# Performance work log

Hardware: AMD Instinct MI355X
Metric: run time of the kernel (lower is better)

Reference implementation:

```python
import jax, jax.numpy as jnp
import numpy as np

GROUP = 64      # quantization group size along the K (in_features) dim
QMAX = 7.0      # symmetric signed int4 range [-7, 7]


def fake_quant_w4a4(t):
    """Per-group symmetric int4 fake-quantization along last dim (STE-friendly).

    t: [..., K] with K % GROUP == 0. Emulates nunchaku's quantize_w4a4
    numerics: scale = max|group| / 7, q = clip(round(t/scale)) * scale.
    """
    shp = t.shape
    g = t.reshape(shp[:-1] + (shp[-1] // GROUP, GROUP))
    scale = jnp.maximum(jnp.max(jnp.abs(g), axis=-1, keepdims=True) / QMAX, 1e-8)
    q = jnp.clip(jnp.round(g / scale), -QMAX, QMAX) * scale
    # straight-through estimator so gradients flow through the quant branch
    q = g + jax.lax.stop_gradient(q - g)
    return q.reshape(shp)


def setup_inputs() -> dict:
    key = jax.random.key(0)
    k0, k1, k2, k3, k4, k5 = jax.random.split(key, 6)
    B, K, N, R = 8192, 2048, 2048, 32  # tokens, in_features, out_features, rank
    x = jax.random.normal(k0, (B, K), jnp.float32)
    residual_weight = jax.random.normal(k1, (N, K), jnp.float32) * 0.02
    lora_down = jax.random.normal(k2, (K, R), jnp.float32) * 0.02
    lora_up = jax.random.normal(k3, (N, R), jnp.float32) * 0.02
    smooth = jax.random.uniform(k4, (K,), jnp.float32, minval=0.5, maxval=2.0)
    bias = jax.random.normal(k5, (N,), jnp.float32) * 0.01
    return {"x": x, "residual_weight": residual_weight, "lora_down": lora_down,
            "lora_up": lora_up, "smooth": smooth, "bias": bias}


def reference(x, residual_weight, lora_down, lora_up, smooth, bias):
    """SVDQuant forward: W4A4 GEMM on the residual weight fused with an
    FP low-rank (SVD) correction and per-channel smoothing.

    y = Q4(x*smooth) @ Q4(W_res).T + (x*smooth) @ lora_down @ lora_up.T + bias
    """
    x_s = x * smooth                                   # [B, K] smoothed activations
    y_lr = (x_s @ lora_down) @ lora_up.T               # [B, R] -> [B, N] low-rank branch
    y_q = fake_quant_w4a4(x_s) @ fake_quant_w4a4(residual_weight).T  # int4xint4 branch
    return y_q + y_lr + bias
```

## Files before the change

kernel.cpp:

```cpp
#include <hip/hip_runtime.h>
#include <stdint.h>


typedef __attribute__((ext_vector_type(8))) short short8;
typedef __attribute__((ext_vector_type(8))) unsigned short ushort8;
typedef __attribute__((ext_vector_type(4))) unsigned short ushort4v;
typedef __attribute__((ext_vector_type(4))) float floatx4;

#define M_TOK 8192
#define K_IN  2048
#define N_OUT 2048
#define RANK  32
#define KC    2080
#define NKT   65
#define XS_STRIDE 2056

__device__ __forceinline__ unsigned short f2bf(float f) {
  unsigned int u = __float_as_uint(f);
  u += 0x7fff + ((u >> 16) & 1);
  return (unsigned short)(u >> 16);
}

__device__ __forceinline__ void quant8(const float* v, unsigned short* q) {
  float amax = 0.f;
#pragma unroll
  for (int i = 0; i < 8; ++i) amax = fmaxf(amax, fabsf(v[i]));
  amax = fmaxf(amax, __shfl_xor(amax, 1, 64));
  amax = fmaxf(amax, __shfl_xor(amax, 2, 64));
  amax = fmaxf(amax, __shfl_xor(amax, 4, 64));
  float scale = fmaxf(amax / 7.0f, 1e-8f);
#pragma unroll
  for (int i = 0; i < 8; ++i) {
    float qq = rintf(v[i] / scale);
    qq = fminf(fmaxf(qq, -7.f), 7.f);
    q[i] = f2bf(qq * scale);
  }
}

__global__ __launch_bounds__(256) void ldt_kernel(const float* __restrict__ ld,
                                                  unsigned short* __restrict__ ldT) {
  int t = threadIdx.x, b = blockIdx.x;
  int r = t & 31, kk = b * 64 + (t >> 5);
#pragma unroll
  for (int i = 0; i < 8; ++i)
    ldT[r * 2048 + kk + i * 8] = f2bf(ld[(size_t)(kk + i * 8) * RANK + r]);
}

__global__ __launch_bounds__(256) void prep_kernel(const float* __restrict__ x,
                                                   const float* __restrict__ smooth,
                                                   const float* __restrict__ wgt,
                                                   const unsigned short* __restrict__ ldT,
                                                   const float* __restrict__ lup,
                                                   unsigned short* __restrict__ Xcat,
                                                   unsigned short* __restrict__ Wcat) {
  __shared__ unsigned short xs[16 * XS_STRIDE];
  __shared__ float red[4][16][32];
  int tid = threadIdx.x;

  if (blockIdx.x >= 512) {
    int row = blockIdx.x - 512;
    const float4* wr = (const float4*)(wgt + (size_t)row * K_IN);
    float4 a0 = wr[tid * 2], a1 = wr[tid * 2 + 1];
    float v[8] = {a0.x, a0.y, a0.z, a0.w, a1.x, a1.y, a1.z, a1.w};
    ushort8 q;
    quant8(v, (unsigned short*)&q);
    *(ushort8*)(Wcat + (size_t)row * KC + tid * 8) = q;
    if (tid < 32) Wcat[(size_t)row * KC + 2048 + tid] = f2bf(lup[row * RANK + tid]);
    return;
  }

  int rowbase = blockIdx.x * 16;
  int w = tid >> 6, lane = tid & 63, quad = lane >> 4, l16 = lane & 15;

  const float4* sr = (const float4*)smooth;
  float4 s0 = sr[tid * 2], s1 = sr[tid * 2 + 1];
#pragma unroll 2
  for (int r = 0; r < 16; ++r) {
    const float4* xr = (const float4*)(x + (size_t)(rowbase + r) * K_IN);
    float4 a0 = xr[tid * 2], a1 = xr[tid * 2 + 1];
    float v[8] = {a0.x * s0.x, a0.y * s0.y, a0.z * s0.z, a0.w * s0.w,
                  a1.x * s1.x, a1.y * s1.y, a1.z * s1.z, a1.w * s1.w};
    ushort8 q;
    quant8(v, (unsigned short*)&q);
    *(ushort8*)(Xcat + (size_t)(rowbase + r) * KC + tid * 8) = q;
    ushort8 sb;
#pragma unroll
    for (int t = 0; t < 8; ++t) sb[t] = f2bf(v[t]);
    *(ushort8*)(xs + r * XS_STRIDE + tid * 8) = sb;
  }
  __syncthreads();

  floatx4 acc[2];
  acc[0] = (floatx4)0.f;
  acc[1] = (floatx4)0.f;
  int kbase = w * 512;
#pragma unroll 2
  for (int it = 0; it < 16; ++it) {
    int k = kbase + it * 32 + quad * 8;
    short8 af = *(const short8*)(xs + l16 * XS_STRIDE + k);
    short8 b0 = *(const short8*)(ldT + (size_t)l16 * 2048 + k);
    short8 b1 = *(const short8*)(ldT + (size_t)(16 + l16) * 2048 + k);
    acc[0] = __builtin_amdgcn_mfma_f32_16x16x32_bf16(af, b0, acc[0], 0, 0, 0);
    acc[1] = __builtin_amdgcn_mfma_f32_16x16x32_bf16(af, b1, acc[1], 0, 0, 0);
  }
#pragma unroll
  for (int nt = 0; nt < 2; ++nt)
#pragma unroll
    for (int r = 0; r < 4; ++r)
      red[w][quad * 4 + r][nt * 16 + l16] = acc[nt][r];
  __syncthreads();
  if (tid < 128) {
    int rl = tid >> 3, seg = tid & 7;
    ushort4v o;
#pragma unroll
    for (int j = 0; j < 4; ++j) {
      int c = seg * 4 + j;
      float s = red[0][rl][c] + red[1][rl][c] + red[2][rl][c] + red[3][rl][c];
      o[j] = f2bf(s);
    }
    *(ushort4v*)(Xcat + (size_t)(rowbase + rl) * KC + 2048 + seg * 4) = o;
  }
}

__device__ __forceinline__ void gld_lds16(const unsigned short* g, unsigned short* l) {
  __builtin_amdgcn_global_load_lds(
      (const __attribute__((address_space(1))) unsigned int*)g,
      (__attribute__((address_space(3))) unsigned int*)l, 16, 0, 0);
}

__global__ __launch_bounds__(512) void gemm_kernel(const unsigned short* __restrict__ Xcat,
                                                   const unsigned short* __restrict__ Wcat,
                                                   const float* __restrict__ bias,
                                                   float* __restrict__ out) {
  __shared__ unsigned short smem[49152];
  int tid = threadIdx.x;
  int w = tid >> 6, lane = tid & 63, quad = lane >> 4, l16 = lane & 15;
  int wm = w >> 2, wn = w & 3;

  int bid = blockIdx.x;
  int wg = (bid & 7) * 32 + (bid >> 3);
  int bM = (wg >> 3) * 256;
  int bN = (wg & 7) * 256;

  int rowA = tid >> 2;
  int csrc = (tid & 3) ^ ((tid >> 3) & 3);
  const unsigned short* Ag = Xcat + (size_t)(bM + rowA) * KC + csrc * 8;
  const unsigned short* Bg = Wcat + (size_t)(bN + rowA) * KC + csrc * 8;
  int ldsA = w * 512;
  int ldsB = 8192 + w * 512;

#define STAGE(k0, cbuf)                                                      \
  do {                                                                       \
    gld_lds16(Ag + (k0),            smem + (cbuf) + ldsA);                   \
    gld_lds16(Ag + 128 * KC + (k0), smem + (cbuf) + 4096 + ldsA);            \
    gld_lds16(Bg + (k0),            smem + (cbuf) + ldsB);                   \
    gld_lds16(Bg + 128 * KC + (k0), smem + (cbuf) + 4096 + ldsB);            \
  } while (0)

  int cx = (quad ^ ((l16 >> 1) & 3)) * 8;
  int aoff = (wm * 128 + l16) * 32 + cx;
  int boff = 8192 + (wn * 64 + l16) * 32 + cx;

  floatx4 acc[8][4];
#pragma unroll
  for (int mt = 0; mt < 8; ++mt)
#pragma unroll
    for (int nt = 0; nt < 4; ++nt) acc[mt][nt] = (floatx4)0.f;

  int c0 = 0, c1 = 16384, c2 = 32768;

  STAGE(0, c0);
  STAGE(32, c1);
  asm volatile("s_waitcnt vmcnt(4)" ::: "memory");
  __builtin_amdgcn_s_barrier();

  for (int t = 0; t < NKT; ++t) {
    if (t + 2 < NKT) STAGE((t + 2) * 32, c2);

    short8 a[8], b[4];
#pragma unroll
    for (int mt = 0; mt < 8; ++mt) a[mt] = *(const short8*)(smem + c0 + aoff + mt * 512);
#pragma unroll
    for (int nt = 0; nt < 4; ++nt) b[nt] = *(const short8*)(smem + c0 + boff + nt * 512);

    __builtin_amdgcn_s_setprio(1);
#pragma unroll
    for (int mt = 0; mt < 8; ++mt)
#pragma unroll
      for (int nt = 0; nt < 4; ++nt)
        acc[mt][nt] = __builtin_amdgcn_mfma_f32_16x16x32_bf16(a[mt], b[nt],
                                                              acc[mt][nt], 0, 0, 0);
    __builtin_amdgcn_s_setprio(0);

    if (t < NKT - 2)
      asm volatile("s_waitcnt vmcnt(4)" ::: "memory");
    else
      asm volatile("s_waitcnt vmcnt(0)" ::: "memory");
    __builtin_amdgcn_s_barrier();
    int tmp = c0; c0 = c1; c1 = c2; c2 = tmp;
  }
#undef STAGE

#pragma unroll
  for (int nt = 0; nt < 4; ++nt) {
    int col = bN + wn * 64 + nt * 16 + l16;
    float bv = bias[col];
#pragma unroll
    for (int mt = 0; mt < 8; ++mt) {
      int row = bM + wm * 128 + mt * 16 + quad * 4;
#pragma unroll
      for (int r2 = 0; r2 < 4; ++r2)
        out[(size_t)(row + r2) * N_OUT + col] = acc[mt][nt][r2] + bv;
    }
  }
}

extern "C" void kernel_launch(void* const* d_in, const int* in_sizes, int n_in,
                              void* d_out, int out_size, void* d_ws, size_t ws_size,
                              hipStream_t stream) {
  const float* x      = (const float*)d_in[0];
  const float* wgt    = (const float*)d_in[1];
  const float* ld     = (const float*)d_in[2];
  const float* lup    = (const float*)d_in[3];
  const float* smooth = (const float*)d_in[4];
  const float* bias   = (const float*)d_in[5];
  float* out = (float*)d_out;

  unsigned short* Xcat = (unsigned short*)d_ws;
  unsigned short* Wcat = Xcat + (size_t)M_TOK * KC;
  unsigned short* ldT  = Wcat + (size_t)N_OUT * KC;

  hipLaunchKernelGGL(ldt_kernel, dim3(K_IN / 64), dim3(256), 0, stream, ld, ldT);
  hipLaunchKernelGGL(prep_kernel, dim3(512 + N_OUT), dim3(256), 0, stream,
                     x, smooth, wgt, ldT, lup, Xcat, Wcat);
  hipLaunchKernelGGL(gemm_kernel, dim3((M_TOK / 256) * (N_OUT / 256)), dim3(512), 0, stream,
                     Xcat, Wcat, bias, out);
}
```

Before: 214.4 us.

## Use 64-wide K tiles with double buffering and ping-pong interleaved MFMA phases

The GEMM K tile grows from 32 to 64, so the concatenated K dimension is padded to 2112 with zeroed tail columns written by the prep kernel. Staging moves to two 64KB buffers with an 8-way XOR swizzle. The loop body is split into four barrier-separated phases that load fragments and then issue MFMAs under raised priority, in a ping-pong style meant to overlap LDS reads and compute across waves. The aim is fewer loop iterations and less barrier/wait overhead per FLOP. The cost is more LDS use, which limits occupancy, many extra barriers, and a little padding compute.

```diff
diff --git a/kernel.cpp b/kernel.cpp
--- a/kernel.cpp
+++ b/kernel.cpp
@@ -11,8 +11,8 @@
 #define K_IN  2048
 #define N_OUT 2048
 #define RANK  32
-#define KC    2080
-#define NKT   65
+#define KC    2112
+#define NTILE 33
 #define XS_STRIDE 2056
 
 __device__ __forceinline__ unsigned short f2bf(float f) {
@@ -39,11 +39,9 @@
 
 __global__ __launch_bounds__(256) void ldt_kernel(const float* __restrict__ ld,
                                                   unsigned short* __restrict__ ldT) {
-  int t = threadIdx.x, b = blockIdx.x;
-  int r = t & 31, kk = b * 64 + (t >> 5);
-#pragma unroll
-  for (int i = 0; i < 8; ++i)
-    ldT[r * 2048 + kk + i * 8] = f2bf(ld[(size_t)(kk + i * 8) * RANK + r]);
+  int g = blockIdx.x * 256 + threadIdx.x;
+  int r = g >> 11, kk = g & 2047;
+  ldT[(size_t)r * 2048 + kk] = f2bf(ld[(size_t)kk * RANK + r]);
 }
 
 __global__ __launch_bounds__(256) void prep_kernel(const float* __restrict__ x,
@@ -65,7 +63,8 @@
     ushort8 q;
     quant8(v, (unsigned short*)&q);
     *(ushort8*)(Wcat + (size_t)row * KC + tid * 8) = q;
-    if (tid < 32) Wcat[(size_t)row * KC + 2048 + tid] = f2bf(lup[row * RANK + tid]);
+    if (tid < 32)      Wcat[(size_t)row * KC + 2048 + tid] = f2bf(lup[row * RANK + tid]);
+    else if (tid < 64) Wcat[(size_t)row * KC + 2048 + tid] = 0;
     return;
   }
 
@@ -88,6 +87,7 @@
     for (int t = 0; t < 8; ++t) sb[t] = f2bf(v[t]);
     *(ushort8*)(xs + r * XS_STRIDE + tid * 8) = sb;
   }
+  *(unsigned int*)(Xcat + (size_t)(rowbase + (tid >> 4)) * KC + 2080 + (tid & 15) * 2) = 0u;
   __syncthreads();
 
   floatx4 acc[2];
@@ -132,7 +132,7 @@
                                                    const unsigned short* __restrict__ Wcat,
                                                    const float* __restrict__ bias,
                                                    float* __restrict__ out) {
-  __shared__ unsigned short smem[49152];
+  __shared__ unsigned short smem[65536];
   int tid = threadIdx.x;
   int w = tid >> 6, lane = tid & 63, quad = lane >> 4, l16 = lane & 15;
   int wm = w >> 2, wn = w & 3;
@@ -142,24 +142,33 @@
   int bM = (wg >> 3) * 256;
   int bN = (wg & 7) * 256;
 
-  int rowA = tid >> 2;
-  int csrc = (tid & 3) ^ ((tid >> 3) & 3);
-  const unsigned short* Ag = Xcat + (size_t)(bM + rowA) * KC + csrc * 8;
-  const unsigned short* Bg = Wcat + (size_t)(bN + rowA) * KC + csrc * 8;
-  int ldsA = w * 512;
-  int ldsB = 8192 + w * 512;
-
-#define STAGE(k0, cbuf)                                                      \
-  do {                                                                       \
-    gld_lds16(Ag + (k0),            smem + (cbuf) + ldsA);                   \
-    gld_lds16(Ag + 128 * KC + (k0), smem + (cbuf) + 4096 + ldsA);            \
-    gld_lds16(Bg + (k0),            smem + (cbuf) + ldsB);                   \
-    gld_lds16(Bg + 128 * KC + (k0), smem + (cbuf) + 4096 + ldsB);            \
+  int srow = tid >> 3;
+  int csrc = (tid & 7) ^ (srow & 7);
+  const unsigned short* Ag = Xcat + (size_t)(bM + srow) * KC + csrc * 8;
+  const unsigned short* Bg = Wcat + (size_t)(bN + srow) * KC + csrc * 8;
+  int ldsrow = w * 512;
+
+#define STAGE(tt, OFF)                                                        \
+  do {                                                                        \
+    int k0_ = (tt) * 64;                                                      \
+    gld_lds16(Ag + k0_,            smem + (OFF) + ldsrow);                    \
+    gld_lds16(Ag + 64 * KC + k0_,  smem + (OFF) + 4096 + ldsrow);             \
+    gld_lds16(Ag + 128 * KC + k0_, smem + (OFF) + 8192 + ldsrow);             \
+    gld_lds16(Ag + 192 * KC + k0_, smem + (OFF) + 12288 + ldsrow);            \
+    gld_lds16(Bg + k0_,            smem + (OFF) + 16384 + ldsrow);            \
+    gld_lds16(Bg + 64 * KC + k0_,  smem + (OFF) + 20480 + ldsrow);            \
+    gld_lds16(Bg + 128 * KC + k0_, smem + (OFF) + 24576 + ldsrow);            \
+    gld_lds16(Bg + 192 * KC + k0_, smem + (OFF) + 28672 + ldsrow);            \
   } while (0)
 
-  int cx = (quad ^ ((l16 >> 1) & 3)) * 8;
-  int aoff = (wm * 128 + l16) * 32 + cx;
-  int boff = 8192 + (wn * 64 + l16) * 32 + cx;
+  int l7 = l16 & 7;
+  int ck0 = (quad ^ l7) * 8;
+  int ck1 = ((4 + quad) ^ l7) * 8;
+  int aoff[8], boff[4];
+#pragma unroll
+  for (int mt = 0; mt < 8; ++mt) aoff[mt] = (wm * 128 + mt * 16 + l16) * 64;
+#pragma unroll
+  for (int nt = 0; nt < 4; ++nt) boff[nt] = 16384 + (wn * 64 + nt * 16 + l16) * 64;
 
   floatx4 acc[8][4];
 #pragma unroll
@@ -167,37 +176,75 @@
 #pragma unroll
     for (int nt = 0; nt < 4; ++nt) acc[mt][nt] = (floatx4)0.f;
 
-  int c0 = 0, c1 = 16384, c2 = 32768;
-
-  STAGE(0, c0);
-  STAGE(32, c1);
-  asm volatile("s_waitcnt vmcnt(4)" ::: "memory");
+  STAGE(0, 0);
+  STAGE(1, 32768);
+  asm volatile("s_waitcnt vmcnt(8)" ::: "memory");
   __builtin_amdgcn_s_barrier();
 
-  for (int t = 0; t < NKT; ++t) {
-    if (t + 2 < NKT) STAGE((t + 2) * 32, c2);
-
-    short8 a[8], b[4];
-#pragma unroll
-    for (int mt = 0; mt < 8; ++mt) a[mt] = *(const short8*)(smem + c0 + aoff + mt * 512);
-#pragma unroll
-    for (int nt = 0; nt < 4; ++nt) b[nt] = *(const short8*)(smem + c0 + boff + nt * 512);
-
-    __builtin_amdgcn_s_setprio(1);
-#pragma unroll
-    for (int mt = 0; mt < 8; ++mt)
-#pragma unroll
-      for (int nt = 0; nt < 4; ++nt)
-        acc[mt][nt] = __builtin_amdgcn_mfma_f32_16x16x32_bf16(a[mt], b[nt],
-                                                              acc[mt][nt], 0, 0, 0);
-    __builtin_amdgcn_s_setprio(0);
-
-    if (t < NKT - 2)
-      asm volatile("s_waitcnt vmcnt(4)" ::: "memory");
-    else
+#pragma unroll 1
+  for (int t = 0; t < NTILE; ++t) {
+    unsigned short* sb = smem + (t & 1) * 32768;
+    short8 a[4], b0[4], b1[4];
+
+#pragma unroll
+    for (int mt = 0; mt < 4; ++mt) a[mt] = *(const short8*)(sb + aoff[mt] + ck0);
+#pragma unroll
+    for (int nt = 0; nt < 4; ++nt) b0[nt] = *(const short8*)(sb + boff[nt] + ck0);
+    __builtin_amdgcn_s_barrier();
+    __builtin_amdgcn_s_setprio(1);
+#pragma unroll
+    for (int mt = 0; mt < 4; ++mt)
+#pragma unroll
+      for (int nt = 0; nt < 4; ++nt)
+        acc[mt][nt] = __builtin_amdgcn_mfma_f32_16x16x32_bf16(a[mt], b0[nt], acc[mt][nt], 0, 0, 0);
+    __builtin_amdgcn_s_setprio(0);
+    __builtin_amdgcn_s_barrier();
+
+#pragma unroll
+    for (int mt = 0; mt < 4; ++mt) a[mt] = *(const short8*)(sb + aoff[mt] + ck1);
+#pragma unroll
+    for (int nt = 0; nt < 4; ++nt) b1[nt] = *(const short8*)(sb + boff[nt] + ck1);
+    __builtin_amdgcn_s_barrier();
+    __builtin_amdgcn_s_setprio(1);
+#pragma unroll
+    for (int mt = 0; mt < 4; ++mt)
+#pragma unroll
+      for (int nt = 0; nt < 4; ++nt)
+        acc[mt][nt] = __builtin_amdgcn_mfma_f32_16x16x32_bf16(a[mt], b1[nt], acc[mt][nt], 0, 0, 0);
+    __builtin_amdgcn_s_setprio(0);
+    __builtin_amdgcn_s_barrier();
+
+#pragma unroll
+    for (int mt = 0; mt < 4; ++mt) a[mt] = *(const short8*)(sb + aoff[mt + 4] + ck0);
+    __builtin_amdgcn_s_barrier();
+    __builtin_amdgcn_s_setprio(1);
+#pragma unroll
+    for (int mt = 0; mt < 4; ++mt)
+#pragma unroll
+      for (int nt = 0; nt < 4; ++nt)
+        acc[mt + 4][nt] = __builtin_amdgcn_mfma_f32_16x16x32_bf16(a[mt], b0[nt], acc[mt + 4][nt], 0, 0, 0);
+    __builtin_amdgcn_s_setprio(0);
+    __builtin_amdgcn_s_barrier();
+
+#pragma unroll
+    for (int mt = 0; mt < 4; ++mt) a[mt] = *(const short8*)(sb + aoff[mt + 4] + ck1);
+    __builtin_amdgcn_s_barrier();
+    __builtin_amdgcn_s_setprio(1);
+#pragma unroll
+    for (int mt = 0; mt < 4; ++mt)
+#pragma unroll
+      for (int nt = 0; nt < 4; ++nt)
+        acc[mt + 4][nt] = __builtin_amdgcn_mfma_f32_16x16x32_bf16(a[mt], b1[nt], acc[mt + 4][nt], 0, 0, 0);
+    __builtin_amdgcn_s_setprio(0);
+    __builtin_amdgcn_s_barrier();
+
+    if (t + 2 < NTILE) {
+      STAGE(t + 2, (t & 1) * 32768);
+      asm volatile("s_waitcnt vmcnt(8)" ::: "memory");
+    } else if (t == NTILE - 2) {
       asm volatile("s_waitcnt vmcnt(0)" ::: "memory");
-    __builtin_amdgcn_s_barrier();
-    int tmp = c0; c0 = c1; c1 = c2; c2 = tmp;
+    }
+    __builtin_amdgcn_s_barrier();
   }
 #undef STAGE
 
@@ -230,7 +277,7 @@
   unsigned short* Wcat = Xcat + (size_t)M_TOK * KC;
   unsigned short* ldT  = Wcat + (size_t)N_OUT * KC;
 
-  hipLaunchKernelGGL(ldt_kernel, dim3(K_IN / 64), dim3(256), 0, stream, ld, ldT);
+  hipLaunchKernelGGL(ldt_kernel, dim3(256), dim3(256), 0, stream, ld, ldT);
   hipLaunchKernelGGL(prep_kernel, dim3(512 + N_OUT), dim3(256), 0, stream,
                      x, smooth, wgt, ldT, lup, Xcat, Wcat);
   hipLaunchKernelGGL(gemm_kernel, dim3((M_TOK / 256) * (N_OUT / 256)), dim3(512), 0, stream,
```

After: 219.0 us. 2.2% more time.

## Split GEMM k-step into two half-phases interleaving loads with MFMA, pad K

Applied to the files above, without the earlier changes.

Restructures the GEMM main loop so each k-tile is processed in two halves. A-tile and B-tile global-to-LDS loads are issued separately between the halves, with extra barriers, to spread memory traffic across compute and reduce register pressure from holding eight A fragments at once. K is padded from 2080 to 2112 (66 tiles, with zeroed padding) for alignment. The prep kernel is also split into separate weight and activation kernels, and the transpose kernel is simplified. The extra barriers and the added k-tile of zeros add overhead.

```diff
diff --git a/kernel.cpp b/kernel.cpp
--- a/kernel.cpp
+++ b/kernel.cpp
@@ -11,8 +11,8 @@
 #define K_IN  2048
 #define N_OUT 2048
 #define RANK  32
-#define KC    2080
-#define NKT   65
+#define KC    2112
+#define NTILE 66
 #define XS_STRIDE 2056
 
 __device__ __forceinline__ unsigned short f2bf(float f) {
@@ -39,42 +39,39 @@
 
 __global__ __launch_bounds__(256) void ldt_kernel(const float* __restrict__ ld,
                                                   unsigned short* __restrict__ ldT) {
-  int t = threadIdx.x, b = blockIdx.x;
-  int r = t & 31, kk = b * 64 + (t >> 5);
-#pragma unroll
-  for (int i = 0; i < 8; ++i)
-    ldT[r * 2048 + kk + i * 8] = f2bf(ld[(size_t)(kk + i * 8) * RANK + r]);
-}
-
-__global__ __launch_bounds__(256) void prep_kernel(const float* __restrict__ x,
-                                                   const float* __restrict__ smooth,
-                                                   const float* __restrict__ wgt,
-                                                   const unsigned short* __restrict__ ldT,
-                                                   const float* __restrict__ lup,
-                                                   unsigned short* __restrict__ Xcat,
-                                                   unsigned short* __restrict__ Wcat) {
+  int g = blockIdx.x * 256 + threadIdx.x;
+  int r = g >> 11, kk = g & 2047;
+  ldT[(size_t)r * 2048 + kk] = f2bf(ld[(size_t)kk * RANK + r]);
+}
+
+__global__ __launch_bounds__(256) void wprep_kernel(const float* __restrict__ wgt,
+                                                    const float* __restrict__ lup,
+                                                    unsigned short* __restrict__ Wcat) {
+  int tid = threadIdx.x;
+  int row = blockIdx.x;
+  const float4* wr = (const float4*)(wgt + (size_t)row * K_IN);
+  float4 a0 = wr[tid * 2], a1 = wr[tid * 2 + 1];
+  float v[8] = {a0.x, a0.y, a0.z, a0.w, a1.x, a1.y, a1.z, a1.w};
+  ushort8 q;
+  quant8(v, (unsigned short*)&q);
+  *(ushort8*)(Wcat + (size_t)row * KC + tid * 8) = q;
+  if (tid < 32)      Wcat[(size_t)row * KC + 2048 + tid] = f2bf(lup[row * RANK + tid]);
+  else if (tid < 64) Wcat[(size_t)row * KC + 2048 + tid] = 0;
+}
+
+__global__ __launch_bounds__(256) void xprep_kernel(const float* __restrict__ x,
+                                                    const float* __restrict__ smooth,
+                                                    const unsigned short* __restrict__ ldT,
+                                                    unsigned short* __restrict__ Xcat) {
   __shared__ unsigned short xs[16 * XS_STRIDE];
   __shared__ float red[4][16][32];
   int tid = threadIdx.x;
-
-  if (blockIdx.x >= 512) {
-    int row = blockIdx.x - 512;
-    const float4* wr = (const float4*)(wgt + (size_t)row * K_IN);
-    float4 a0 = wr[tid * 2], a1 = wr[tid * 2 + 1];
-    float v[8] = {a0.x, a0.y, a0.z, a0.w, a1.x, a1.y, a1.z, a1.w};
-    ushort8 q;
-    quant8(v, (unsigned short*)&q);
-    *(ushort8*)(Wcat + (size_t)row * KC + tid * 8) = q;
-    if (tid < 32) Wcat[(size_t)row * KC + 2048 + tid] = f2bf(lup[row * RANK + tid]);
-    return;
-  }
-
   int rowbase = blockIdx.x * 16;
   int w = tid >> 6, lane = tid & 63, quad = lane >> 4, l16 = lane & 15;
 
   const float4* sr = (const float4*)smooth;
   float4 s0 = sr[tid * 2], s1 = sr[tid * 2 + 1];
-#pragma unroll 2
+#pragma unroll 4
   for (int r = 0; r < 16; ++r) {
     const float4* xr = (const float4*)(x + (size_t)(rowbase + r) * K_IN);
     float4 a0 = xr[tid * 2], a1 = xr[tid * 2 + 1];
@@ -88,6 +85,7 @@
     for (int t = 0; t < 8; ++t) sb[t] = f2bf(v[t]);
     *(ushort8*)(xs + r * XS_STRIDE + tid * 8) = sb;
   }
+  *(unsigned int*)(Xcat + (size_t)(rowbase + (tid >> 4)) * KC + 2080 + (tid & 15) * 2) = 0u;
   __syncthreads();
 
   floatx4 acc[2];
@@ -142,64 +140,88 @@
   int bM = (wg >> 3) * 256;
   int bN = (wg & 7) * 256;
 
-  int rowA = tid >> 2;
+  int srow = tid >> 2;
   int csrc = (tid & 3) ^ ((tid >> 3) & 3);
-  const unsigned short* Ag = Xcat + (size_t)(bM + rowA) * KC + csrc * 8;
-  const unsigned short* Bg = Wcat + (size_t)(bN + rowA) * KC + csrc * 8;
-  int ldsA = w * 512;
-  int ldsB = 8192 + w * 512;
-
-#define STAGE(k0, cbuf)                                                      \
-  do {                                                                       \
-    gld_lds16(Ag + (k0),            smem + (cbuf) + ldsA);                   \
-    gld_lds16(Ag + 128 * KC + (k0), smem + (cbuf) + 4096 + ldsA);            \
-    gld_lds16(Bg + (k0),            smem + (cbuf) + ldsB);                   \
-    gld_lds16(Bg + 128 * KC + (k0), smem + (cbuf) + 4096 + ldsB);            \
+  const unsigned short* Ag = Xcat + (size_t)(bM + srow) * KC + csrc * 8;
+  const unsigned short* Bg = Wcat + (size_t)(bN + srow) * KC + csrc * 8;
+  int ldsw = w * 512;
+
+  int ck = (quad ^ ((l16 >> 1) & 3)) * 8;
+  int aoff[8], boff[4];
+#pragma unroll
+  for (int mt = 0; mt < 8; ++mt) aoff[mt] = (wm * 128 + mt * 16 + l16) * 32 + ck;
+#pragma unroll
+  for (int nt = 0; nt < 4; ++nt) boff[nt] = 8192 + (wn * 64 + nt * 16 + l16) * 32 + ck;
+
+  floatx4 acc[8][4];
+#pragma unroll
+  for (int mt = 0; mt < 8; ++mt)
+#pragma unroll
+    for (int nt = 0; nt < 4; ++nt) acc[mt][nt] = (floatx4)0.f;
+
+  int b0 = 0, b1 = 16384, b2 = 32768;
+
+#define STAGE_A(tt, OFF)                                                      \
+  do {                                                                        \
+    int k0_ = (tt) * 32;                                                      \
+    gld_lds16(Ag + k0_,           smem + (OFF) + ldsw);                       \
+    gld_lds16(Ag + 128 * KC + k0_, smem + (OFF) + 4096 + ldsw);               \
   } while (0)
-
-  int cx = (quad ^ ((l16 >> 1) & 3)) * 8;
-  int aoff = (wm * 128 + l16) * 32 + cx;
-  int boff = 8192 + (wn * 64 + l16) * 32 + cx;
-
-  floatx4 acc[8][4];
-#pragma unroll
-  for (int mt = 0; mt < 8; ++mt)
-#pragma unroll
-    for (int nt = 0; nt < 4; ++nt) acc[mt][nt] = (floatx4)0.f;
-
-  int c0 = 0, c1 = 16384, c2 = 32768;
-
-  STAGE(0, c0);
-  STAGE(32, c1);
+#define STAGE_B(tt, OFF)                                                      \
+  do {                                                                        \
+    int k0_ = (tt) * 32;                                                      \
+    gld_lds16(Bg + k0_,           smem + (OFF) + 8192 + ldsw);                \
+    gld_lds16(Bg + 128 * KC + k0_, smem + (OFF) + 12288 + ldsw);              \
+  } while (0)
+
+  STAGE_A(0, 0);
+  STAGE_B(0, 0);
+  STAGE_A(1, 16384);
+  STAGE_B(1, 16384);
   asm volatile("s_waitcnt vmcnt(4)" ::: "memory");
   __builtin_amdgcn_s_barrier();
 
-  for (int t = 0; t < NKT; ++t) {
-    if (t + 2 < NKT) STAGE((t + 2) * 32, c2);
-
-    short8 a[8], b[4];
-#pragma unroll
-    for (int mt = 0; mt < 8; ++mt) a[mt] = *(const short8*)(smem + c0 + aoff + mt * 512);
-#pragma unroll
-    for (int nt = 0; nt < 4; ++nt) b[nt] = *(const short8*)(smem + c0 + boff + nt * 512);
-
+#pragma unroll 1
+  for (int t = 0; t < NTILE; ++t) {
+    unsigned short* sb = smem + b0;
+    short8 a[4], b[4];
+
+#pragma unroll
+    for (int mt = 0; mt < 4; ++mt) a[mt] = *(const short8*)(sb + aoff[mt]);
+#pragma unroll
+    for (int nt = 0; nt < 4; ++nt) b[nt] = *(const short8*)(sb + boff[nt]);
+    if (t + 2 < NTILE) STAGE_A(t + 2, b2);
+    __builtin_amdgcn_s_barrier();
     __builtin_amdgcn_s_setprio(1);
 #pragma unroll
-    for (int mt = 0; mt < 8; ++mt)
+    for (int mt = 0; mt < 4; ++mt)
 #pragma unroll
       for (int nt = 0; nt < 4; ++nt)
-        acc[mt][nt] = __builtin_amdgcn_mfma_f32_16x16x32_bf16(a[mt], b[nt],
-                                                              acc[mt][nt], 0, 0, 0);
+        acc[mt][nt] = __builtin_amdgcn_mfma_f32_16x16x32_bf16(a[mt], b[nt], acc[mt][nt], 0, 0, 0);
     __builtin_amdgcn_s_setprio(0);
-
-    if (t < NKT - 2)
+    __builtin_amdgcn_s_barrier();
+
+#pragma unroll
+    for (int mt = 0; mt < 4; ++mt) a[mt] = *(const short8*)(sb + aoff[mt + 4]);
+    if (t + 2 < NTILE) STAGE_B(t + 2, b2);
+    __builtin_amdgcn_s_barrier();
+    __builtin_amdgcn_s_setprio(1);
+#pragma unroll
+    for (int mt = 0; mt < 4; ++mt)
+#pragma unroll
+      for (int nt = 0; nt < 4; ++nt)
+        acc[mt + 4][nt] = __builtin_amdgcn_mfma_f32_16x16x32_bf16(a[mt], b[nt], acc[mt + 4][nt], 0, 0, 0);
+    __builtin_amdgcn_s_setprio(0);
+
+    if (t < NTILE - 2)
       asm volatile("s_waitcnt vmcnt(4)" ::: "memory");
-    else
+    else if (t == NTILE - 2)
       asm volatile("s_waitcnt vmcnt(0)" ::: "memory");
     __builtin_amdgcn_s_barrier();
-    int tmp = c0; c0 = c1; c1 = c2; c2 = tmp;
-  }
-#undef STAGE
+    int tmp = b0; b0 = b1; b1 = b2; b2 = tmp;
+  }
+#undef STAGE_A
+#undef STAGE_B
 
 #pragma unroll
   for (int nt = 0; nt < 4; ++nt) {
@@ -230,9 +252,10 @@
   unsigned short* Wcat = Xcat + (size_t)M_TOK * KC;
   unsigned short* ldT  = Wcat + (size_t)N_OUT * KC;
 
-  hipLaunchKernelGGL(ldt_kernel, dim3(K_IN / 64), dim3(256), 0, stream, ld, ldT);
-  hipLaunchKernelGGL(prep_kernel, dim3(512 + N_OUT), dim3(256), 0, stream,
-                     x, smooth, wgt, ldT, lup, Xcat, Wcat);
+  hipLaunchKernelGGL(ldt_kernel, dim3(256), dim3(256), 0, stream, ld, ldT);
+  hipLaunchKernelGGL(wprep_kernel, dim3(N_OUT), dim3(256), 0, stream, wgt, lup, Wcat);
+  hipLaunchKernelGGL(xprep_kernel, dim3(M_TOK / 16), dim3(256), 0, stream,
+                     x, smooth, ldT, Xcat);
   hipLaunchKernelGGL(gemm_kernel, dim3((M_TOK / 256) * (N_OUT / 256)), dim3(512), 0, stream,
                      Xcat, Wcat, bias, out);
 }
```

After: 218.8 us. 1.02x slower.
